# Performance work log

Measured on AMD Instinct MI355X. Metric: run time of the kernel, lower is better.

The kernel has to match this reference:

```python
import jax, jax.numpy as jnp
from jax import lax
import numpy as np

NF = 64      # feature channels
G = 8        # mask groups
NBR = 3      # top-k neighbors
PATCH = 7    # correlation patch size (patches[0])
CORK = 3     # correlation / unfold kernel size
PAD_COR = 1  # (CORK-1)//2
PAD_S = 4    # PAD_COR + (PATCH-1)//2
ADD = 6      # 2*PAD_S - CORK + 1
B, H, W = 4, 96, 96


def leaky(x):
    return jnp.where(x >= 0, x, 0.1 * x)


def _conv(x, w, b, pad):
    y = lax.conv_general_dilated(x, w, (1, 1), [(pad[0], pad[0]), (pad[1], pad[1])],
                                 dimension_numbers=('NCHW', 'OIHW', 'NCHW'))
    return y + b[None, :, None, None]


def _normalize(x, eps=1e-12):
    n = jnp.sqrt(jnp.sum(x * x, axis=1, keepdims=True))
    return x / jnp.maximum(n, eps)


def _correlation(f1, f2):
    # spatial-correlation-sampler: kernel=3, patch=7, stride=1, pad=1, dilations=1
    # out[b, ph*7+pw, i, j] = sum_{c,u,v} f1p[b,c,i+u,j+v] * f2p[b,c,i+u+ph-3, j+v+pw-3]
    # (unnormalized; only topk indices are consumed downstream, so any positive
    #  constant scale is irrelevant)
    Bx, C, Hx, Wx = f1.shape
    f1p = jnp.pad(f1, ((0, 0), (0, 0), (PAD_COR, PAD_COR), (PAD_COR, PAD_COR)))
    f2p = jnp.pad(f2, ((0, 0), (0, 0), (PAD_S, PAD_S), (PAD_S, PAD_S)))
    outs = []
    for ph in range(PATCH):
        for pw in range(PATCH):
            s = jnp.sum(f1p * f2p[:, :, ph:ph + Hx + 2, pw:pw + Wx + 2], axis=1)  # [B,H+2,W+2]
            o = sum(s[:, u:u + Hx, v:v + Wx] for u in range(CORK) for v in range(CORK))
            outs.append(o)
    return jnp.stack(outs, axis=1)  # [B, 49, H, W]


def setup_inputs() -> dict:
    key = jax.random.key(0)
    ks = jax.random.split(key, 16)

    def wt(k, shape):
        fan_in = shape[1] * shape[2] * shape[3]
        return jax.random.normal(k, shape, jnp.float32) * (1.0 / np.sqrt(fan_in))

    return {
        'ref_fea_l': jax.random.normal(ks[0], (B, NF, H, W), jnp.float32),
        'w1': wt(ks[1], (NF, NF * 2, 3, 3)), 'b1': jnp.zeros((NF,), jnp.float32),
        'w2': wt(ks[2], (NF, NF, 3, 3)),     'b2': jnp.zeros((NF,), jnp.float32),
        'w3': wt(ks[3], (NF, NF, 7, 1)),     'b3': jnp.zeros((NF,), jnp.float32),
        'w4': wt(ks[4], (NF, NF, 1, 7)),     'b4': jnp.zeros((NF,), jnp.float32),
        'wm': wt(ks[5], (G * CORK ** 2, NF, 3, 3)), 'bm': jnp.zeros((G * CORK ** 2,), jnp.float32),
        'wnn': wt(ks[6], (NF, NF * NBR, 3, 3)), 'bnn': jnp.zeros((NF,), jnp.float32),
        'wf': wt(ks[7], (NF, NF * 2, 3, 3)),    'bf': jnp.zeros((NF,), jnp.float32),
    }


def reference(ref_fea_l, w1, b1, w2, b2, w3, b3, w4, b4, wm, bm, wnn, bnn, wf, bf):
    Bx, C, Hx, Wx = ref_fea_l.shape
    nbr_fea = ref_fea_l  # aliased in the original forward

    # mask branch
    x = jnp.concatenate([nbr_fea, ref_fea_l], axis=1)
    x = leaky(_conv(x, w1, b1, (1, 1)))
    x = leaky(_conv(x, w2, b2, (1, 1)))
    x = leaky(_conv(x, w3, b3, (3, 0)))
    x = leaky(_conv(x, w4, b4, (0, 3)))
    mask = _conv(x, wm, bm, (1, 1)).reshape(Bx, G, 1, CORK ** 2, Hx, Wx)

    # correlation + topk neighbor displacements
    nref = _normalize(ref_fea_l)
    corr = _correlation(nref, nref)                     # [B,49,H,W]
    _, idx = lax.top_k(corr.transpose(0, 2, 3, 1), NBR)  # [B,H,W,NBR]

    # flat indices into the (H+6)x(W+6) unfold grid
    ph = idx // PATCH
    pw = idx % PATCH
    yy = jnp.arange(Hx)[:, None, None]
    xx = jnp.arange(Wx)[None, :, None]
    flat = ((ph + yy) * (Wx + ADD) + (pw + xx)).reshape(Bx, Hx * Wx * NBR)

    # unfold (im2col) of nbr features with pad 4, then gather chosen 3x3 patches
    nbr_pad = jnp.pad(nbr_fea, ((0, 0), (0, 0), (PAD_S, PAD_S), (PAD_S, PAD_S)))
    patches = lax.conv_general_dilated_patches(nbr_pad, (CORK, CORK), (1, 1), 'VALID',
                                               dimension_numbers=('NCHW', 'OIHW', 'NCHW'))
    pl = patches.reshape(Bx, C * CORK ** 2, -1).transpose(0, 2, 1)  # [B, (H+6)(W+6), C*9]
    gath = jnp.take_along_axis(pl, flat[:, :, None], axis=1)        # [B, HW*NBR, C*9]
    gath = gath.reshape(Bx * Hx * Wx, NBR * C, CORK, CORK)

    # conv over gathered patches then modulated mask-weighted reduce
    g = leaky(_conv(gath, wnn, bnn, (1, 1)))                         # [BHW, C, 3, 3]
    g = g.reshape(Bx, Hx, Wx, C, CORK ** 2).transpose(0, 3, 4, 1, 2)
    g = g.reshape(Bx, G, C // G, CORK ** 2, Hx, Wx)
    agg = leaky(jnp.sum(g * mask, axis=3).reshape(Bx, C, Hx, Wx))

    out = leaky(_conv(jnp.concatenate([ref_fea_l, agg], axis=1), wf, bf, (1, 1)))
    return out
```

## Files before the change

kernel.cpp:

```cpp
#include <hip/hip_runtime.h>
#include <hip/hip_bf16.h>

constexpr int BATCH = 4;
constexpr int H = 96, W = 96, HW = H * W;
constexpr int NBR = 3;

using bf16x8 = __attribute__((ext_vector_type(8))) short;
using f32x4 = __attribute__((ext_vector_type(4))) float;

static __device__ __forceinline__ float leakyf(float x) {
    return x >= 0.f ? x : 0.1f * x;
}

static __device__ __forceinline__ short f2bf(float x) {
    __hip_bfloat16 h = __float2bfloat16(x);
    return *reinterpret_cast<short*>(&h);
}

static __device__ __forceinline__ float bf2f(short s) {
    __hip_bfloat16 h = *reinterpret_cast<__hip_bfloat16*>(&s);
    return __bfloat162float(h);
}

__global__ __launch_bounds__(256) void k_pre(const float* __restrict__ ref,
                                             short* __restrict__ reft,
                                             float* __restrict__ nrn) {
    int p = blockIdx.x * 256 + threadIdx.x;
    if (p >= BATCH * HW) return;
    int b = p / HW, ij = p % HW;
    const float* src = ref + b * 64 * HW + ij;
    float v[64];
    float ss = 0.f;
#pragma unroll
    for (int c = 0; c < 64; ++c) {
        v[c] = src[c * HW];
        ss += v[c] * v[c];
    }
    float inv = 1.f / fmaxf(sqrtf(ss), 1e-12f);
    short* rd = reft + (size_t)p * 64;
#pragma unroll
    for (int cc = 0; cc < 8; ++cc) {
        bf16x8 o;
#pragma unroll
        for (int j = 0; j < 8; ++j) o[j] = f2bf(v[cc * 8 + j]);
        *(bf16x8*)(rd + cc * 8) = o;
    }
    float* nd = nrn + b * 64 * HW + ij;
#pragma unroll
    for (int c = 0; c < 64; ++c) nd[c * HW] = v[c] * inv;
}

__global__ void k_prep(const float* __restrict__ src, short* __restrict__ dst,
                       int OC, int ICt, int ICsrc, int KH, int KW, int NT,
                       int fold, int total) {
    int i = blockIdx.x * 256 + threadIdx.x;
    if (i >= total) return;
    int e = i & 7, l = (i >> 3) & 63;
    int rest = i >> 9;
    int nt = rest % NT;
    rest /= NT;
    int ICK = ICt >> 5;
    int kk = rest % ICK;
    int tap = rest / ICK;
    int ic = kk * 32 + (l >> 4) * 8 + e;
    int oc = nt * 16 + (l & 15);
    int u = tap / KW, v = tap % KW;
    float val = 0.f;
    if (oc < OC) {
        val = src[((oc * ICsrc + ic) * KH + u) * KW + v];
        if (fold) val += src[((oc * ICsrc + 64 + ic) * KH + u) * KW + v];
    }
    dst[i] = f2bf(val);
}

template <int KH, int KW, int IC, int OC, int OMODE, bool BLDS, int NSPL>
__global__ __launch_bounds__(512) void k_cmfma(
    const short* __restrict__ inA, const short* __restrict__ inB,
    const short* __restrict__ Bp, const float* __restrict__ bias,
    void* __restrict__ outp) {
    constexpr int TI = 8, TJ = 32;
    constexpr int PH = (KH - 1) / 2, PW = (KW - 1) / 2;
    constexpr int LR = TI + KH - 1, LC = TJ + KW - 1;
    constexpr int ICB = IC * 2;
    constexpr int LS = (ICB == 128) ? 7 : 8;
    constexpr int ICK = IC / 32;
    constexpr int NTF = (OC + 15) / 16;
    constexpr int NTb = NTF / NSPL;
    constexpr int TAPS = KH * KW;
    constexpr int NOCT = ICB / 16;
    __shared__ char Xs[LR * LC * ICB];
    __shared__ short Bs[BLDS ? TAPS * ICK * NTb * 512 : 8];
    const int tj0 = blockIdx.x * TJ, ti0 = blockIdx.y * TI;
    const int b = blockIdx.z / NSPL;
    const int nt0 = (blockIdx.z % NSPL) * NTb;
    const int tid = threadIdx.x;
    if (BLDS) {
        for (int u2 = tid; u2 < TAPS * ICK * NTb * 64; u2 += 512) {
            int l2 = u2 & 63;
            int rest = u2 >> 6;
            int nt = rest % NTb;
            int qk = rest / NTb;
            ((bf16x8*)Bs)[u2] = ((const bf16x8*)Bp)[(qk * NTF + nt0 + nt) * 64 + l2];
        }
    }
    for (int u2 = tid; u2 < LR * LC * NOCT; u2 += 512) {
        int oct = u2 % NOCT;
        int hp = u2 / NOCT;
        int hr = hp / LC, hc = hp % LC;
        int gi = ti0 + hr - PH, gj = tj0 + hc - PW;
        bf16x8 v = {};
        if (gi >= 0 && gi < H && gj >= 0 && gj < W) {
            const short* s = (oct < 8) ? inA : inB;
            v = *(const bf16x8*)(s + (size_t)(b * HW + gi * W + gj) * 64 +
                                 (oct & 7) * 8);
        }
        int byte = hp * ICB + oct * 16;
        byte ^= ((byte >> LS) & 7) << 4;
        *(bf16x8*)(Xs + byte) = v;
    }
    __syncthreads();
    const int wave = tid >> 6, l = tid & 63;
    const int r = l & 15, q = l >> 4;
    const int mt0 = wave * 2;
    int p0 = mt0 * 16 + r, p1 = p0 + 16;
    int li0 = p0 >> 5, lj0 = p0 & 31, li1 = p1 >> 5, lj1 = p1 & 31;
    f32x4 acc[2][NTb] = {};
#pragma unroll
    for (int t = 0; t < TAPS; ++t) {
        const int u = t / KW, v = t % KW;
        int hp0 = (li0 + u) * LC + (lj0 + v);
        int hp1 = (li1 + u) * LC + (lj1 + v);
#pragma unroll
        for (int kk = 0; kk < ICK; ++kk) {
            int ab0 = hp0 * ICB + kk * 64 + q * 16;
            ab0 ^= ((ab0 >> LS) & 7) << 4;
            int ab1 = hp1 * ICB + kk * 64 + q * 16;
            ab1 ^= ((ab1 >> LS) & 7) << 4;
            bf16x8 a0 = *(const bf16x8*)(Xs + ab0);
            bf16x8 a1 = *(const bf16x8*)(Xs + ab1);
            const short* bbase =
                BLDS ? (const short*)Bs + (t * ICK + kk) * NTb * 512 + l * 8
                     : Bp + ((t * ICK + kk) * NTF + nt0) * 512 + l * 8;
#pragma unroll
            for (int nt = 0; nt < NTb; ++nt) {
                bf16x8 bv = *(const bf16x8*)(bbase + nt * 512);
                acc[0][nt] =
                    __builtin_amdgcn_mfma_f32_16x16x32_bf16(a0, bv, acc[0][nt], 0, 0, 0);
                acc[1][nt] =
                    __builtin_amdgcn_mfma_f32_16x16x32_bf16(a1, bv, acc[1][nt], 0, 0, 0);
            }
        }
    }
    const int col = l & 15;
#pragma unroll
    for (int mt = 0; mt < 2; ++mt)
#pragma unroll
        for (int nt = 0; nt < NTb; ++nt) {
            int oc = (nt0 + nt) * 16 + col;
            float bs = (oc < OC) ? bias[oc] : 0.f;
#pragma unroll
            for (int j = 0; j < 4; ++j) {
                int p = (mt0 + mt) * 16 + q * 4 + j;
                int gi = ti0 + (p >> 5), gj = tj0 + (p & 31);
                float val = acc[mt][nt][j] + bs;
                if (OMODE == 0) {
                    val = leakyf(val);
                    *((short*)outp + (size_t)(b * HW + gi * W + gj) * 64 + oc) =
                        f2bf(val);
                } else if (OMODE == 1) {
                    if (oc < 72)
                        *((short*)outp + (size_t)(b * HW + gi * W + gj) * 72 + oc) =
                            f2bf(val);
                } else {
                    val = leakyf(val);
                    *((float*)outp + (size_t)(b * 64 + oc) * HW + gi * W + gj) = val;
                }
            }
        }
}

__global__ void k_corr_sym(const float* __restrict__ nr, float* __restrict__ S) {
    int idx = blockIdx.x * 256 + threadIdx.x;
    if (idx >= BATCH * 25 * 98 * 98) return;
    int x = idx % 98;
    int y = (idx / 98) % 98;
    int d = (idx / (98 * 98)) % 25;
    int b = idx / (98 * 98 * 25);
    int dy = d / 7, dx = d % 7;
    int f1i = y - 1, f1j = x - 1;
    int f2i = y + dy - 4, f2j = x + dx - 4;
    float r = 0.f;
    if (f1i >= 0 && f1i < H && f1j >= 0 && f1j < W && f2i >= 0 && f2i < H &&
        f2j >= 0 && f2j < W) {
        const float* p1 = nr + b * 64 * HW + f1i * W + f1j;
        const float* p2 = nr + b * 64 * HW + f2i * W + f2j;
#pragma unroll 16
        for (int c = 0; c < 64; ++c) r = fmaf(p1[c * HW], p2[c * HW], r);
    }
    S[((size_t)(b * 49 + d)) * (98 * 98) + y * 98 + x] = r;
    if (d < 24) {
        int y2 = y + dy - 3, x2 = x + dx - 3;
        if (y2 >= 0 && y2 < 98 && x2 >= 0 && x2 < 98)
            S[((size_t)(b * 49 + 48 - d)) * (98 * 98) + y2 * 98 + x2] = r;
    }
}

__global__ void k_topk(const float* __restrict__ S, int* __restrict__ idx3) {
    int p = blockIdx.x * 256 + threadIdx.x;
    if (p >= BATCH * HW) return;
    int b = p / HW, i = (p % HW) / W, j = p % W;
    float v0 = -1e30f, v1 = -1e30f, v2 = -1e30f;
    int d0 = 0, d1 = 0, d2 = 0;
    for (int d = 0; d < 49; ++d) {
        const float* s = S + ((b * 49 + d) * 98 + i) * 98 + j;
        float v = 0.f;
#pragma unroll
        for (int u = 0; u < 3; ++u)
#pragma unroll
            for (int vv = 0; vv < 3; ++vv) v += s[u * 98 + vv];
        if (v > v0) {
            v2 = v1; d2 = d1; v1 = v0; d1 = d0; v0 = v; d0 = d;
        } else if (v > v1) {
            v2 = v1; d2 = d1; v1 = v; d1 = d;
        } else if (v > v2) {
            v2 = v; d2 = d;
        }
    }
    idx3[p * 3 + 0] = d0;
    idx3[p * 3 + 1] = d1;
    idx3[p * 3 + 2] = d2;
}

__global__ void k_bswz2(const float* __restrict__ wnn, short* __restrict__ B2) {
    int i = blockIdx.x * 256 + threadIdx.x;
    if (i >= 4 * 3 * 2 * 9 * 512) return;
    int e = i & 7, l = (i >> 3) & 63;
    int t = (i >> 9) % 9;
    int h2 = (i / (512 * 9)) % 2;
    int n = (i / (512 * 9 * 2)) % 3;
    int nt = i / (512 * 9 * 2 * 3);
    int oc = nt * 16 + (l & 15);
    int c = h2 * 32 + (l >> 4) * 8 + e;
    int u = t / 3, v = t % 3;
    B2[i] = f2bf(wnn[((oc * 192 + n * 64 + c) * 3 + u) * 3 + v]);
}

__global__ __launch_bounds__(512, 4) void k_agg_mfma(
    const short* __restrict__ refT, const int* __restrict__ idx3,
    const short* __restrict__ B2, const float* __restrict__ bnn,
    const short* __restrict__ maskT, const short* __restrict__ zpad,
    short* __restrict__ agg) {
    constexpr int PX = 32;
    constexpr int BUFB = 36864;
    __shared__ short A_lds[2 * 2 * 18 * 64 * 8];
    __shared__ int sd[PX][NBR];
    const int p0 = blockIdx.x * PX;
    const int b = p0 / HW;
    const int i0 = (p0 % HW) / W;
    const int j0 = p0 % W;
    const int tid = threadIdx.x;
    const int wave = tid >> 6;
    const int lane = tid & 63;
    if (tid < PX * NBR)
        sd[tid / NBR][tid % NBR] = idx3[(p0 + tid / NBR) * NBR + tid % NBR];
    __syncthreads();

    auto STAGE = [&](int n, int buf) {
        for (int r2 = wave; r2 < 36; r2 += 8) {
            int kkl = r2 % 18;
            int ph = r2 / 18;
            int rs = kkl >> 1;
            int oh = kkl & 1;
            int c = lane ^ (((lane >> 4) & 3) | (((buf * 36 + r2) & 1) << 2));
            int oct = oh * 4 + (c >> 4);
            int px = ph * 16 + (c & 15);
            int d = sd[px][n];
            int gi = i0 + d / 7 + rs / 3 - 4;
            int gj = j0 + px + d % 7 + rs % 3 - 4;
            const short* src = (gi >= 0 && gi < H && gj >= 0 && gj < W)
                                   ? refT + (size_t)(b * HW + gi * W + gj) * 64 +
                                         oct * 8
                                   : zpad;
            __builtin_amdgcn_global_load_lds(
                (const __attribute__((address_space(1))) void*)src,
                (__attribute__((address_space(3))) void*)((char*)A_lds +
                                                          buf * BUFB + r2 * 1024),
                16, 0, 0);
        }
    };

    const int w = wave & 3;
    const int half = wave >> 2;
    f32x4 acc[9] = {};
    const short* Bw = B2 + (size_t)w * (3 * 2 * 9 * 512) + lane * 8;

    auto COMPUTE = [&](int n, int buf) {
#pragma unroll
        for (int h2 = 0; h2 < 2; ++h2) {
            const short* bb = Bw + (n * 2 + h2) * 9 * 512;
            bf16x8 bv[9];
#pragma unroll
            for (int t = 0; t < 9; ++t) bv[t] = *(const bf16x8*)(bb + t * 512);
#pragma unroll
            for (int rs = 0; rs < 9; ++rs) {
                int kkl = rs * 2 + h2;
                int ab = buf * BUFB + ((((half * 18 + kkl) << 6) + lane) << 4);
                ab ^= ((ab >> 8) & 7) << 4;
                bf16x8 a = *(const bf16x8*)((char*)A_lds + ab);
#pragma unroll
                for (int t = 0; t < 9; ++t) {
                    const int y = rs / 3 - t / 3 + 1;
                    const int x = rs % 3 - t % 3 + 1;
                    if (y >= 0 && y < 3 && x >= 0 && x < 3)
                        acc[y * 3 + x] = __builtin_amdgcn_mfma_f32_16x16x32_bf16(
                            a, bv[t], acc[y * 3 + x], 0, 0, 0);
                }
            }
        }
    };

    STAGE(0, 0);
    STAGE(1, 1);
    __syncthreads();
    COMPUTE(0, 0);
    __syncthreads();
    STAGE(2, 0);
    COMPUTE(1, 1);
    __syncthreads();
    COMPUTE(2, 0);

    const int oc = w * 16 + (lane & 15);
    const float bn = bnn[oc];
    const int mrow = (lane >> 4) * 4;
#pragma unroll
    for (int j = 0; j < 4; ++j) {
        int px = half * 16 + mrow + j;
        int ij = i0 * W + j0 + px;
        const short* mb = maskT + (size_t)(b * HW + ij) * 72 + (oc >> 3) * 9;
        float sacc = 0.f;
#pragma unroll
        for (int yx = 0; yx < 9; ++yx) {
            float gv = leakyf(acc[yx][j] + bn);
            sacc += gv * bf2f(mb[yx]);
        }
        agg[(size_t)(b * HW + ij) * 64 + oc] = f2bf(leakyf(sacc));
    }
}

extern "C" void kernel_launch(void* const* d_in, const int* in_sizes, int n_in,
                              void* d_out, int out_size, void* d_ws,
                              size_t ws_size, hipStream_t stream) {
    const float* ref = (const float*)d_in[0];
    const float* w1 = (const float*)d_in[1];
    const float* b1 = (const float*)d_in[2];
    const float* w2 = (const float*)d_in[3];
    const float* b2 = (const float*)d_in[4];
    const float* w3 = (const float*)d_in[5];
    const float* b3 = (const float*)d_in[6];
    const float* w4 = (const float*)d_in[7];
    const float* b4 = (const float*)d_in[8];
    const float* wm = (const float*)d_in[9];
    const float* bm = (const float*)d_in[10];
    const float* wnn = (const float*)d_in[11];
    const float* bnn = (const float*)d_in[12];
    const float* wf = (const float*)d_in[13];
    const float* bf = (const float*)d_in[14];

    char* ws = (char*)d_ws;
    constexpr size_t O_NRN = 0;
    constexpr size_t O_S = O_NRN + (size_t)BATCH * HW * 64 * 4;
    constexpr size_t O_REFT = O_S + (size_t)BATCH * 49 * 98 * 98 * 4;
    constexpr size_t O_X1 = O_REFT + (size_t)BATCH * HW * 64 * 2;
    constexpr size_t O_X2 = O_X1 + (size_t)BATCH * HW * 64 * 2;
    constexpr size_t O_MASKT = O_X2 + (size_t)BATCH * HW * 64 * 2;
    constexpr size_t O_IDX = O_MASKT + (size_t)BATCH * HW * 72 * 2;
    constexpr size_t O_P1 = O_IDX + (size_t)BATCH * HW * 3 * 4;
    constexpr size_t O_P2 = O_P1 + 73728 * 2;
    constexpr size_t O_P3 = O_P2 + 73728 * 2;
    constexpr size_t O_P4 = O_P3 + 28672 * 2;
    constexpr size_t O_PM = O_P4 + 28672 * 2;
    constexpr size_t O_PF = O_PM + 46080 * 2;
    constexpr size_t O_ZP = O_PF + 73728 * 2;

    float* NRN = (float*)(ws + O_NRN);
    float* S = (float*)(ws + O_S);
    short* BSWZ2 = (short*)(ws + O_S);
    short* REFT = (short*)(ws + O_REFT);
    short* X1 = (short*)(ws + O_X1);
    short* X2 = (short*)(ws + O_X2);
    short* MASKT = (short*)(ws + O_MASKT);
    int* IDX = (int*)(ws + O_IDX);
    short* P1 = (short*)(ws + O_P1);
    short* P2 = (short*)(ws + O_P2);
    short* P3 = (short*)(ws + O_P3);
    short* P4 = (short*)(ws + O_P4);
    short* PM = (short*)(ws + O_PM);
    short* PF = (short*)(ws + O_PF);
    short* ZPAD = (short*)(ws + O_ZP);

    k_pre<<<(BATCH * HW + 255) / 256, 256, 0, stream>>>(ref, REFT, NRN);
    k_prep<<<144, 256, 0, stream>>>(w1, P1, 64, 64, 128, 3, 3, 4, 1, 36864);
    k_prep<<<144, 256, 0, stream>>>(w2, P2, 64, 64, 64, 3, 3, 4, 0, 36864);
    k_prep<<<112, 256, 0, stream>>>(w3, P3, 64, 64, 64, 7, 1, 4, 0, 28672);
    k_prep<<<112, 256, 0, stream>>>(w4, P4, 64, 64, 64, 1, 7, 4, 0, 28672);
    k_prep<<<180, 256, 0, stream>>>(wm, PM, 72, 64, 64, 3, 3, 5, 0, 46080);
    k_prep<<<288, 256, 0, stream>>>(wf, PF, 64, 128, 128, 3, 3, 4, 0, 73728);

    dim3 cgrid2(3, 12, BATCH * 2);
    dim3 cgrid1(3, 12, BATCH);
    k_cmfma<3, 3, 64, 64, 0, true, 2><<<cgrid2, 512, 0, stream>>>(REFT, nullptr, P1, b1, X1);
    k_cmfma<3, 3, 64, 64, 0, true, 2><<<cgrid2, 512, 0, stream>>>(X1, nullptr, P2, b2, X2);
    k_cmfma<7, 1, 64, 64, 0, true, 2><<<cgrid2, 512, 0, stream>>>(X2, nullptr, P3, b3, X1);
    k_cmfma<1, 7, 64, 64, 0, true, 2><<<cgrid2, 512, 0, stream>>>(X1, nullptr, P4, b4, X2);
    k_cmfma<3, 3, 64, 72, 1, true, 1><<<cgrid1, 512, 0, stream>>>(X2, nullptr, PM, bm, MASKT);

    for (int b = 0; b < BATCH; ++b)
        hipMemsetAsync(S + ((size_t)(b * 49 + 25)) * 98 * 98,
                       0, (size_t)24 * 98 * 98 * 4, stream);
    hipMemsetAsync(ZPAD, 0, 16, stream);
    k_corr_sym<<<(BATCH * 25 * 98 * 98 + 255) / 256, 256, 0, stream>>>(NRN, S);
    k_topk<<<BATCH * HW / 256, 256, 0, stream>>>(S, IDX);

    k_bswz2<<<432, 256, 0, stream>>>(wnn, BSWZ2);

    k_agg_mfma<<<BATCH * HW / 32, 512, 0, stream>>>(REFT, IDX, BSWZ2, bnn, MASKT,
                                                    ZPAD, X1);

    k_cmfma<3, 3, 128, 64, 2, false, 1><<<cgrid1, 512, 0, stream>>>(REFT, X1, PF, bf, d_out);
}
```

Before: 209.0 us.

## Merge weight-prep launches, fold memsets into correlation, split mask/final convs

Replaces seven weight-packing launches, the wnn swizzle kernel and two rounds of memsets with one combined prep kernel that also zeroes the pad buffer. The correlation kernel now computes two adjacent pixels per thread with float2 loads and writes the zeros for the mirrored half itself, so the separate memsets go away. The mask conv and the final conv are split across more output-channel blocks (NSPL 5 and 2) for more parallelism. In the aggregation kernel, neighbor offsets are precomputed once into shared memory. The intent is fewer launches and better occupancy, at the cost of more divergent branches and possibly redundant input staging per block.

New measurement: 215.7 us. +3.2%, slower.

```diff
diff --git a/kernel.cpp b/kernel.cpp
--- a/kernel.cpp
+++ b/kernel.cpp
@@ -50,11 +50,10 @@
     for (int c = 0; c < 64; ++c) nd[c * HW] = v[c] * inv;
 }
 
-__global__ void k_prep(const float* __restrict__ src, short* __restrict__ dst,
-                       int OC, int ICt, int ICsrc, int KH, int KW, int NT,
-                       int fold, int total) {
-    int i = blockIdx.x * 256 + threadIdx.x;
-    if (i >= total) return;
+static __device__ __forceinline__ void packw(const float* __restrict__ src,
+                                             short* __restrict__ dst, int i,
+                                             int OC, int ICt, int ICsrc, int KH,
+                                             int KW, int NT, int fold) {
     int e = i & 7, l = (i >> 3) & 63;
     int rest = i >> 9;
     int nt = rest % NT;
@@ -71,6 +70,51 @@
         if (fold) val += src[((oc * ICsrc + 64 + ic) * KH + u) * KW + v];
     }
     dst[i] = f2bf(val);
+}
+
+constexpr int E1 = 36864, E2 = 36864, E3 = 28672, E4 = 28672, E5 = 46080,
+              E6 = 73728, E7 = 110592;
+constexpr int C1 = E1, C2 = C1 + E2, C3 = C2 + E3, C4 = C3 + E4, C5 = C4 + E5,
+              C6 = C5 + E6, C7 = C6 + E7, CT = C7 + 8;
+__global__ void k_prep_all(const float* __restrict__ w1,
+                           const float* __restrict__ w2,
+                           const float* __restrict__ w3,
+                           const float* __restrict__ w4,
+                           const float* __restrict__ wm,
+                           const float* __restrict__ wf,
+                           const float* __restrict__ wnn,
+                           short* __restrict__ P1, short* __restrict__ P2,
+                           short* __restrict__ P3, short* __restrict__ P4,
+                           short* __restrict__ PM, short* __restrict__ PF,
+                           short* __restrict__ B2, short* __restrict__ zpad) {
+    int i = blockIdx.x * 256 + threadIdx.x;
+    if (i >= CT) return;
+    if (i < C1) {
+        packw(w1, P1, i, 64, 64, 128, 3, 3, 4, 1);
+    } else if (i < C2) {
+        packw(w2, P2, i - C1, 64, 64, 64, 3, 3, 4, 0);
+    } else if (i < C3) {
+        packw(w3, P3, i - C2, 64, 64, 64, 7, 1, 4, 0);
+    } else if (i < C4) {
+        packw(w4, P4, i - C3, 64, 64, 64, 1, 7, 4, 0);
+    } else if (i < C5) {
+        packw(wm, PM, i - C4, 72, 64, 64, 3, 3, 5, 0);
+    } else if (i < C6) {
+        packw(wf, PF, i - C5, 64, 128, 128, 3, 3, 4, 0);
+    } else if (i < C7) {
+        int j = i - C6;
+        int e = j & 7, l = (j >> 3) & 63;
+        int t = (j >> 9) % 9;
+        int h2 = (j / (512 * 9)) % 2;
+        int n = (j / (512 * 9 * 2)) % 3;
+        int nt = j / (512 * 9 * 2 * 3);
+        int oc = nt * 16 + (l & 15);
+        int c = h2 * 32 + (l >> 4) * 8 + e;
+        int u = t / 3, v = t % 3;
+        B2[j] = f2bf(wnn[((oc * 192 + n * 64 + c) * 3 + u) * 3 + v]);
+    } else {
+        zpad[i - C7] = 0;
+    }
 }
 
 template <int KH, int KW, int IC, int OC, int OMODE, bool BLDS, int NSPL>
@@ -179,29 +223,64 @@
         }
 }
 
-__global__ void k_corr_sym(const float* __restrict__ nr, float* __restrict__ S) {
+__global__ void k_corr2(const float* __restrict__ nr, float* __restrict__ S) {
     int idx = blockIdx.x * 256 + threadIdx.x;
-    if (idx >= BATCH * 25 * 98 * 98) return;
-    int x = idx % 98;
-    int y = (idx / 98) % 98;
-    int d = (idx / (98 * 98)) % 25;
-    int b = idx / (98 * 98 * 25);
+    if (idx >= BATCH * 49 * 98 * 49) return;
+    int xp = idx % 49, x0 = xp * 2, x1 = x0 + 1;
+    int y = (idx / 49) % 98;
+    int d = (idx / (49 * 98)) % 49;
+    int b = idx / (49 * 98 * 49);
     int dy = d / 7, dx = d % 7;
-    int f1i = y - 1, f1j = x - 1;
-    int f2i = y + dy - 4, f2j = x + dx - 4;
-    float r = 0.f;
-    if (f1i >= 0 && f1i < H && f1j >= 0 && f1j < W && f2i >= 0 && f2i < H &&
-        f2j >= 0 && f2j < W) {
-        const float* p1 = nr + b * 64 * HW + f1i * W + f1j;
-        const float* p2 = nr + b * 64 * HW + f2i * W + f2j;
+    float* row = S + ((size_t)(b * 49 + d)) * (98 * 98) + y * 98;
+    if (d > 24) {
+        int yy = y + dy - 3;
+        if (yy < 0 || yy >= 98) {
+            row[x0] = 0.f;
+            row[x1] = 0.f;
+        } else {
+            if (x0 + dx - 3 < 0 || x0 + dx - 3 >= 98) row[x0] = 0.f;
+            if (x1 + dx - 3 < 0 || x1 + dx - 3 >= 98) row[x1] = 0.f;
+        }
+        return;
+    }
+    int f1i = y - 1, f2i = y + dy - 4;
+    float r0 = 0.f, r1 = 0.f;
+    if (f1i >= 0 && f1i < H && f2i >= 0 && f2i < H) {
+        int f1j0 = x0 - 1, f2j0 = x0 + dx - 4;
+        bool v0 = f1j0 >= 0 && f1j0 < W && f2j0 >= 0 && f2j0 < W;
+        bool v1 = f1j0 + 1 >= 0 && f1j0 + 1 < W && f2j0 + 1 >= 0 && f2j0 + 1 < W;
+        const float* p1 = nr + (size_t)b * 64 * HW + f1i * W + f1j0;
+        const float* p2 = nr + (size_t)b * 64 * HW + f2i * W + f2j0;
+        if (v0 && v1) {
 #pragma unroll 16
-        for (int c = 0; c < 64; ++c) r = fmaf(p1[c * HW], p2[c * HW], r);
-    }
-    S[((size_t)(b * 49 + d)) * (98 * 98) + y * 98 + x] = r;
+            for (int c = 0; c < 64; ++c) {
+                float2 a = *(const float2*)(p1 + c * HW);
+                float2 q = *(const float2*)(p2 + c * HW);
+                r0 = fmaf(a.x, q.x, r0);
+                r1 = fmaf(a.y, q.y, r1);
+            }
+        } else {
+            if (v0) {
+#pragma unroll 16
+                for (int c = 0; c < 64; ++c) r0 = fmaf(p1[c * HW], p2[c * HW], r0);
+            }
+            if (v1) {
+#pragma unroll 16
+                for (int c = 0; c < 64; ++c)
+                    r1 = fmaf(p1[1 + c * HW], p2[1 + c * HW], r1);
+            }
+        }
+    }
+    row[x0] = r0;
+    row[x1] = r1;
     if (d < 24) {
-        int y2 = y + dy - 3, x2 = x + dx - 3;
-        if (y2 >= 0 && y2 < 98 && x2 >= 0 && x2 < 98)
-            S[((size_t)(b * 49 + 48 - d)) * (98 * 98) + y2 * 98 + x2] = r;
+        int y2 = y + dy - 3;
+        if (y2 >= 0 && y2 < 98) {
+            float* mrow = S + ((size_t)(b * 49 + 48 - d)) * (98 * 98) + y2 * 98;
+            int x20 = x0 + dx - 3;
+            if (x20 >= 0 && x20 < 98) mrow[x20] = r0;
+            if (x20 + 1 >= 0 && x20 + 1 < 98) mrow[x20 + 1] = r1;
+        }
     }
 }
 
@@ -231,20 +310,6 @@
     idx3[p * 3 + 2] = d2;
 }
 
-__global__ void k_bswz2(const float* __restrict__ wnn, short* __restrict__ B2) {
-    int i = blockIdx.x * 256 + threadIdx.x;
-    if (i >= 4 * 3 * 2 * 9 * 512) return;
-    int e = i & 7, l = (i >> 3) & 63;
-    int t = (i >> 9) % 9;
-    int h2 = (i / (512 * 9)) % 2;
-    int n = (i / (512 * 9 * 2)) % 3;
-    int nt = i / (512 * 9 * 2 * 3);
-    int oc = nt * 16 + (l & 15);
-    int c = h2 * 32 + (l >> 4) * 8 + e;
-    int u = t / 3, v = t % 3;
-    B2[i] = f2bf(wnn[((oc * 192 + n * 64 + c) * 3 + u) * 3 + v]);
-}
-
 __global__ __launch_bounds__(512, 4) void k_agg_mfma(
     const short* __restrict__ refT, const int* __restrict__ idx3,
     const short* __restrict__ B2, const float* __restrict__ bnn,
@@ -253,7 +318,7 @@
     constexpr int PX = 32;
     constexpr int BUFB = 36864;
     __shared__ short A_lds[2 * 2 * 18 * 64 * 8];
-    __shared__ int sd[PX][NBR];
+    __shared__ short sgi[PX][NBR], sgj[PX][NBR];
     const int p0 = blockIdx.x * PX;
     const int b = p0 / HW;
     const int i0 = (p0 % HW) / W;
@@ -261,8 +326,12 @@
     const int tid = threadIdx.x;
     const int wave = tid >> 6;
     const int lane = tid & 63;
-    if (tid < PX * NBR)
-        sd[tid / NBR][tid % NBR] = idx3[(p0 + tid / NBR) * NBR + tid % NBR];
+    if (tid < PX * NBR) {
+        int px = tid / NBR, n = tid % NBR;
+        int d = idx3[(p0 + px) * NBR + n];
+        sgi[px][n] = (short)(i0 + d / 7 - 4);
+        sgj[px][n] = (short)(j0 + px + d % 7 - 4);
+    }
     __syncthreads();
 
     auto STAGE = [&](int n, int buf) {
@@ -274,9 +343,8 @@
             int c = lane ^ (((lane >> 4) & 3) | (((buf * 36 + r2) & 1) << 2));
             int oct = oh * 4 + (c >> 4);
             int px = ph * 16 + (c & 15);
-            int d = sd[px][n];
-            int gi = i0 + d / 7 + rs / 3 - 4;
-            int gj = j0 + px + d % 7 + rs % 3 - 4;
+            int gi = sgi[px][n] + rs / 3;
+            int gj = sgj[px][n] + rs % 3;
             const short* src = (gi >= 0 && gi < H && gj >= 0 && gj < W)
                                    ? refT + (size_t)(b * HW + gi * W + gj) * 64 +
                                          oct * 8
@@ -375,16 +443,16 @@
     constexpr size_t O_MASKT = O_X2 + (size_t)BATCH * HW * 64 * 2;
     constexpr size_t O_IDX = O_MASKT + (size_t)BATCH * HW * 72 * 2;
     constexpr size_t O_P1 = O_IDX + (size_t)BATCH * HW * 3 * 4;
-    constexpr size_t O_P2 = O_P1 + 73728 * 2;
-    constexpr size_t O_P3 = O_P2 + 73728 * 2;
-    constexpr size_t O_P4 = O_P3 + 28672 * 2;
-    constexpr size_t O_PM = O_P4 + 28672 * 2;
-    constexpr size_t O_PF = O_PM + 46080 * 2;
-    constexpr size_t O_ZP = O_PF + 73728 * 2;
+    constexpr size_t O_P2 = O_P1 + (size_t)E1 * 2;
+    constexpr size_t O_P3 = O_P2 + (size_t)E2 * 2;
+    constexpr size_t O_P4 = O_P3 + (size_t)E3 * 2;
+    constexpr size_t O_PM = O_P4 + (size_t)E4 * 2;
+    constexpr size_t O_PF = O_PM + (size_t)E5 * 2;
+    constexpr size_t O_B2 = O_PF + (size_t)E6 * 2;
+    constexpr size_t O_ZP = O_B2 + (size_t)E7 * 2;
 
     float* NRN = (float*)(ws + O_NRN);
     float* S = (float*)(ws + O_S);
-    short* BSWZ2 = (short*)(ws + O_S);
     short* REFT = (short*)(ws + O_REFT);
     short* X1 = (short*)(ws + O_X1);
     short* X2 = (short*)(ws + O_X2);
@@ -396,35 +464,27 @@
     short* P4 = (short*)(ws + O_P4);
     short* PM = (short*)(ws + O_PM);
     short* PF = (short*)(ws + O_PF);
+    short* B2 = (short*)(ws + O_B2);
     short* ZPAD = (short*)(ws + O_ZP);
 
     k_pre<<<(BATCH * HW + 255) / 256, 256, 0, stream>>>(ref, REFT, NRN);
-    k_prep<<<144, 256, 0, stream>>>(w1, P1, 64, 64, 128, 3, 3, 4, 1, 36864);
-    k_prep<<<144, 256, 0, stream>>>(w2, P2, 64, 64, 64, 3, 3, 4, 0, 36864);
-    k_prep<<<112, 256, 0, stream>>>(w3, P3, 64, 64, 64, 7, 1, 4, 0, 28672);
-    k_prep<<<112, 256, 0, stream>>>(w4, P4, 64, 64, 64, 1, 7, 4, 0, 28672);
-    k_prep<<<180, 256, 0, stream>>>(wm, PM, 72, 64, 64, 3, 3, 5, 0, 46080);
-    k_prep<<<288, 256, 0, stream>>>(wf, PF, 64, 128, 128, 3, 3, 4, 0, 73728);
+    k_prep_all<<<(CT + 255) / 256, 256, 0, stream>>>(w1, w2, w3, w4, wm, wf, wnn,
+                                                     P1, P2, P3, P4, PM, PF, B2,
+                                                     ZPAD);
 
     dim3 cgrid2(3, 12, BATCH * 2);
-    dim3 cgrid1(3, 12, BATCH);
+    dim3 cgrid5(3, 12, BATCH * 5);
     k_cmfma<3, 3, 64, 64, 0, true, 2><<<cgrid2, 512, 0, stream>>>(REFT, nullptr, P1, b1, X1);
     k_cmfma<3, 3, 64, 64, 0, true, 2><<<cgrid2, 512, 0, stream>>>(X1, nullptr, P2, b2, X2);
     k_cmfma<7, 1, 64, 64, 0, true, 2><<<cgrid2, 512, 0, stream>>>(X2, nullptr, P3, b3, X1);
     k_cmfma<1, 7, 64, 64, 0, true, 2><<<cgrid2, 512, 0, stream>>>(X1, nullptr, P4, b4, X2);
-    k_cmfma<3, 3, 64, 72, 1, true, 1><<<cgrid1, 512, 0, stream>>>(X2, nullptr, PM, bm, MASKT);
-
-    for (int b = 0; b < BATCH; ++b)
-        hipMemsetAsync(S + ((size_t)(b * 49 + 25)) * 98 * 98,
-                       0, (size_t)24 * 98 * 98 * 4, stream);
-    hipMemsetAsync(ZPAD, 0, 16, stream);
-    k_corr_sym<<<(BATCH * 25 * 98 * 98 + 255) / 256, 256, 0, stream>>>(NRN, S);
+    k_cmfma<3, 3, 64, 72, 1, true, 5><<<cgrid5, 512, 0, stream>>>(X2, nullptr, PM, bm, MASKT);
+
+    k_corr2<<<(BATCH * 49 * 98 * 49 + 255) / 256, 256, 0, stream>>>(NRN, S);
     k_topk<<<BATCH * HW / 256, 256, 0, stream>>>(S, IDX);
 
-    k_bswz2<<<432, 256, 0, stream>>>(wnn, BSWZ2);
-
-    k_agg_mfma<<<BATCH * HW / 32, 512, 0, stream>>>(REFT, IDX, BSWZ2, bnn, MASKT,
+    k_agg_mfma<<<BATCH * HW / 32, 512, 0, stream>>>(REFT, IDX, B2, bnn, MASKT,
                                                     ZPAD, X1);
 
-    k_cmfma<3, 3, 128, 64, 2, false, 1><<<cgrid1, 512, 0, stream>>>(REFT, X1, PF, bf, d_out);
-}
+    k_cmfma<3, 3, 128, 64, 2, false, 2><<<cgrid2, 512, 0, stream>>>(REFT, X1, PF, bf, d_out);
+}
```
